# Optimization experiments

Hardware: AMD Instinct MI355X
Metric: run time of the kernel (lower is better)

Reference implementation:

```python
import jax, jax.numpy as jnp
import numpy as np

IN_FEATURES = 4096
OUT_FEATURES = 11008
PACK_COLS = IN_FEATURES // 2
BATCH, SEQ = 2, 2048


def setup_inputs() -> dict:
    key = jax.random.key(0)
    k_x, k_w, k_s, k_b = jax.random.split(key, 4)
    x = jax.random.normal(k_x, (BATCH, SEQ, IN_FEATURES), dtype=jnp.float32)
    # packed uint8 values (two int4 nibbles per byte), stored as int32 in [0, 256)
    weight_packed = jax.random.randint(k_w, (OUT_FEATURES, PACK_COLS), 0, 256, dtype=jnp.int32)
    # per-output-row dequant scale (abs_max/7 in the original); small positive values
    scale = jax.random.uniform(k_s, (OUT_FEATURES,), dtype=jnp.float32, minval=0.001, maxval=0.02)
    bias = jax.random.normal(k_b, (OUT_FEATURES,), dtype=jnp.float32)
    return {"x": x, "weight_packed": weight_packed, "scale": scale, "bias": bias}


def _dequantize(weight_packed, scale):
    # low nibble stored first (even columns), high nibble second (odd columns)
    lo = (weight_packed & 15) - 8          # [out, pack_cols] int32 in [-8, 7]
    hi = ((weight_packed >> 4) & 15) - 8   # [out, pack_cols]
    # interleave lo/hi -> [out, 2*pack_cols] matching w[:, 0::2]=lo, w[:, 1::2]=hi
    w_int = jnp.stack([lo, hi], axis=-1).reshape(OUT_FEATURES, 2 * PACK_COLS)
    w_int = w_int[:, :IN_FEATURES]
    return w_int.astype(jnp.float32) * scale[:, None]  # [out, in] fp32


def reference(x, weight_packed, scale, bias):
    w = _dequantize(weight_packed, scale)                 # [out, in]
    # F.linear: x @ w.T + bias
    return jnp.einsum('bsi,oi->bso', x, w) + bias
```

## Files before the change

kernel.cpp:

```cpp
#include <hip/hip_runtime.h>
#include <hip/hip_fp16.h>

#define M_TOTAL 4096
#define N_TOTAL 11008
#define K_TOTAL 4096
#define KPACK   2048

typedef _Float16 f16x4 __attribute__((ext_vector_type(4)));
typedef _Float16 f16x8 __attribute__((ext_vector_type(8)));
typedef float    f32x4 __attribute__((ext_vector_type(4)));

__device__ __forceinline__ void load16_to_lds(const void* g, void* l) {
    __builtin_amdgcn_global_load_lds(
        (const __attribute__((address_space(1))) unsigned int*)g,
        (__attribute__((address_space(3))) unsigned int*)l,
        16, 0, 0);
}

__global__ __launch_bounds__(256)
void _Int4Linear_cvt_x(const float* __restrict__ x, _Float16* __restrict__ xf) {
    const size_t i = ((size_t)blockIdx.x * 256 + threadIdx.x) * 8;
    const float4 v0 = *(const float4*)(x + i);
    const float4 v1 = *(const float4*)(x + i + 4);
    f16x8 h = { (_Float16)v0.x, (_Float16)v0.y, (_Float16)v0.z, (_Float16)v0.w,
                (_Float16)v1.x, (_Float16)v1.y, (_Float16)v1.z, (_Float16)v1.w };
    *(f16x8*)(xf + i) = h;
}

__global__ __launch_bounds__(256)
void _Int4Linear_dequant_w(const int* __restrict__ wp, _Float16* __restrict__ wf) {
    const size_t i = ((size_t)blockIdx.x * 256 + threadIdx.x) * 4;
    const int4 p = *(const int4*)(wp + i);
    const int v[4] = { p.x, p.y, p.z, p.w };
    f16x8 h;
    #pragma unroll
    for (int j = 0; j < 4; ++j) {
        h[2 * j]     = (_Float16)(( v[j]       & 15) - 8);
        h[2 * j + 1] = (_Float16)(((v[j] >> 4) & 15) - 8);
    }
    *(f16x8*)(wf + i * 2) = h;
}

#define BM 256
#define BN 256
#define NKT 64

__global__ __launch_bounds__(512, 2)
void _Int4Linear_54631984005366_kernel(const _Float16* __restrict__ A,
                                       const _Float16* __restrict__ B,
                                       const float* __restrict__ scale,
                                       const float* __restrict__ bias,
                                       float*       __restrict__ out)
{
    extern __shared__ char sm[];
    char* const smA = sm;
    char* const smB = sm + 65536;

    const int t    = threadIdx.x;
    const int wave = t >> 6;
    const int lane = t & 63;
    const int l16  = lane & 15;
    const int quad = lane >> 4;
    const int wm   = wave >> 2;
    const int wn   = wave & 3;

    const int b0 = blockIdx.x;
    const int sw = (b0 & 7) * 86 + (b0 >> 3);
    const int mBase = (sw & 15) * BM;
    const int nBase = (sw >> 4) * BN;

    const int srow = wave * 16 + (lane >> 2);
    const int scol = (((lane & 3) ^ ((lane >> 3) & 3)) << 3);
    const _Float16* const Ab = A + (size_t)(mBase + srow) * K_TOTAL + scol;
    const _Float16* const Bb = B + (size_t)(nBase + srow) * K_TOTAL + scol;
    const int ldst = wave * 1024;

    const int chA  = (quad ^ ((l16 >> 1) & 3)) << 4;
    const int aoff = (wm * 128 + l16) * 64 + chA;
    const int boff = (wn * 64  + l16) * 64 + chA;

    f32x4 acc[8][4] = {};

    #pragma unroll
    for (int r = 0; r < 2; ++r) load16_to_lds(Ab + (size_t)r * 128 * K_TOTAL,      smA + r * 8192 + ldst);
    #pragma unroll
    for (int r = 0; r < 2; ++r) load16_to_lds(Bb + (size_t)r * 128 * K_TOTAL,      smB + r * 8192 + ldst);
    #pragma unroll
    for (int r = 0; r < 2; ++r) load16_to_lds(Ab + (size_t)r * 128 * K_TOTAL + 32, smA + 16384 + r * 8192 + ldst);
    #pragma unroll
    for (int r = 0; r < 2; ++r) load16_to_lds(Bb + (size_t)r * 128 * K_TOTAL + 32, smB + 16384 + r * 8192 + ldst);
    asm volatile("s_waitcnt vmcnt(4)" ::: "memory");
    __builtin_amdgcn_s_barrier();
    __builtin_amdgcn_sched_barrier(0);

    #pragma unroll 2
    for (int t0 = 0; t0 < NKT; ++t0) {
        const int par = (t0 & 1) * 2;
        const int nxp = ((t0 + 1) & 1) * 2;
        const int tn  = (t0 < NKT - 1) ? (t0 + 1) : t0;
        const int kn  = tn * 64;
        char* const Ac0 = smA + (par    ) * 16384;
        char* const Ac1 = smA + (par + 1) * 16384;
        char* const Bc0 = smB + (par    ) * 16384;
        char* const Bc1 = smB + (par + 1) * 16384;
        char* const An0 = smA + (nxp    ) * 16384;
        char* const An1 = smA + (nxp + 1) * 16384;
        char* const Bn0 = smB + (nxp    ) * 16384;
        char* const Bn1 = smB + (nxp + 1) * 16384;

        {
            #pragma unroll
            for (int r = 0; r < 2; ++r) load16_to_lds(Ab + (size_t)r * 128 * K_TOTAL + kn, An0 + r * 8192 + ldst);
            #pragma unroll
            for (int r = 0; r < 2; ++r) load16_to_lds(Bb + (size_t)r * 128 * K_TOTAL + kn, Bn0 + r * 8192 + ldst);
            f16x8 a[8], b[4];
            #pragma unroll
            for (int f = 0; f < 8; ++f) a[f] = *(const f16x8*)(Ac0 + aoff + f * 1024);
            #pragma unroll
            for (int f = 0; f < 4; ++f) b[f] = *(const f16x8*)(Bc0 + boff + f * 1024);
            __builtin_amdgcn_s_setprio(1);
            #pragma unroll
            for (int mf = 0; mf < 8; ++mf)
                #pragma unroll
                for (int nf = 0; nf < 4; ++nf)
                    acc[mf][nf] = __builtin_amdgcn_mfma_f32_16x16x32_f16(a[mf], b[nf], acc[mf][nf], 0, 0, 0);
            __builtin_amdgcn_s_setprio(0);
            asm volatile("s_waitcnt vmcnt(4)" ::: "memory");
            __builtin_amdgcn_s_barrier();
            __builtin_amdgcn_sched_barrier(0);
        }

        {
            #pragma unroll
            for (int r = 0; r < 2; ++r) load16_to_lds(Ab + (size_t)r * 128 * K_TOTAL + kn + 32, An1 + r * 8192 + ldst);
            #pragma unroll
            for (int r = 0; r < 2; ++r) load16_to_lds(Bb + (size_t)r * 128 * K_TOTAL + kn + 32, Bn1 + r * 8192 + ldst);
            f16x8 a[8], b[4];
            #pragma unroll
            for (int f = 0; f < 8; ++f) a[f] = *(const f16x8*)(Ac1 + aoff + f * 1024);
            #pragma unroll
            for (int f = 0; f < 4; ++f) b[f] = *(const f16x8*)(Bc1 + boff + f * 1024);
            __builtin_amdgcn_s_setprio(1);
            #pragma unroll
            for (int mf = 0; mf < 8; ++mf)
                #pragma unroll
                for (int nf = 0; nf < 4; ++nf)
                    acc[mf][nf] = __builtin_amdgcn_mfma_f32_16x16x32_f16(a[mf], b[nf], acc[mf][nf], 0, 0, 0);
            __builtin_amdgcn_s_setprio(0);
            asm volatile("s_waitcnt vmcnt(4)" ::: "memory");
            __builtin_amdgcn_s_barrier();
            __builtin_amdgcn_sched_barrier(0);
        }
    }
    asm volatile("s_waitcnt vmcnt(0)" ::: "memory");

    #pragma unroll
    for (int nf = 0; nf < 4; ++nf) {
        const int n = nBase + wn * 64 + nf * 16 + l16;
        const float s  = scale[n];
        const float bz = bias[n];
        #pragma unroll
        for (int mf = 0; mf < 8; ++mf) {
            const int mb = mBase + wm * 128 + mf * 16 + quad * 4;
            #pragma unroll
            for (int r = 0; r < 4; ++r)
                out[(size_t)(mb + r) * N_TOTAL + n] = acc[mf][nf][r] * s + bz;
        }
    }
}

#define FBM 128
#define FBN 128
#define FBK 32
#define LDR 40
__global__ __launch_bounds__(256)
void _Int4Linear_fallback(const float* __restrict__ x, const int* __restrict__ wp,
                          const float* __restrict__ scale, const float* __restrict__ bias,
                          float* __restrict__ out)
{
    __shared__ _Float16 As[FBM * LDR];
    __shared__ _Float16 Bs[FBN * LDR];
    const int t = threadIdx.x, wave = t >> 6, lane = t & 63;
    const int l16 = lane & 15, quad = lane >> 4;
    const int nBase = blockIdx.x * FBN, mBase = blockIdx.y * FBM;
    const int wm = (wave >> 1) * 64, wn = (wave & 1) * 64;
    f32x4 acc[4][4] = {};
    for (int k0 = 0; k0 < K_TOTAL; k0 += FBK) {
        #pragma unroll
        for (int i = 0; i < 4; ++i) {
            const int li = i * 256 + t, row = li >> 3, c4 = li & 7;
            const float4 v = *(const float4*)(&x[(size_t)(mBase + row) * K_TOTAL + k0 + c4 * 4]);
            f16x4 hv = { (_Float16)v.x, (_Float16)v.y, (_Float16)v.z, (_Float16)v.w };
            *(f16x4*)(&As[row * LDR + c4 * 4]) = hv;
        }
        #pragma unroll
        for (int i = 0; i < 2; ++i) {
            const int li = i * 256 + t, row = li >> 2, c4 = li & 3;
            const int4 p = *(const int4*)(&wp[(size_t)(nBase + row) * KPACK + (k0 >> 1) + c4 * 4]);
            const int vals[4] = { p.x, p.y, p.z, p.w };
            f16x8 hv;
            #pragma unroll
            for (int j = 0; j < 4; ++j) {
                hv[2 * j]     = (_Float16)(( vals[j]       & 15) - 8);
                hv[2 * j + 1] = (_Float16)(((vals[j] >> 4) & 15) - 8);
            }
            *(f16x8*)(&Bs[row * LDR + c4 * 8]) = hv;
        }
        __syncthreads();
        f16x8 a[4], b[4];
        #pragma unroll
        for (int mt = 0; mt < 4; ++mt)
            a[mt] = *(const f16x8*)(&As[(wm + mt * 16 + l16) * LDR + quad * 8]);
        #pragma unroll
        for (int nt = 0; nt < 4; ++nt)
            b[nt] = *(const f16x8*)(&Bs[(wn + nt * 16 + l16) * LDR + quad * 8]);
        #pragma unroll
        for (int mt = 0; mt < 4; ++mt)
            #pragma unroll
            for (int nt = 0; nt < 4; ++nt)
                acc[mt][nt] = __builtin_amdgcn_mfma_f32_16x16x32_f16(a[mt], b[nt], acc[mt][nt], 0, 0, 0);
        __syncthreads();
    }
    #pragma unroll
    for (int nt = 0; nt < 4; ++nt) {
        const int n = nBase + wn + nt * 16 + l16;
        const float s = scale[n], bz = bias[n];
        #pragma unroll
        for (int mt = 0; mt < 4; ++mt)
            #pragma unroll
            for (int r = 0; r < 4; ++r)
                out[(size_t)(mBase + wm + mt * 16 + quad * 4 + r) * N_TOTAL + n] = acc[mt][nt][r] * s + bz;
    }
}

extern "C" void kernel_launch(void* const* d_in, const int* in_sizes, int n_in,
                              void* d_out, int out_size, void* d_ws, size_t ws_size,
                              hipStream_t stream) {
    const float* x     = (const float*)d_in[0];
    const int*   wp    = (const int*)d_in[1];
    const float* scale = (const float*)d_in[2];
    const float* bias  = (const float*)d_in[3];
    float*       out   = (float*)d_out;

    const size_t xf_bytes = (size_t)M_TOTAL * K_TOTAL * 2;
    const size_t wf_bytes = (size_t)N_TOTAL * K_TOTAL * 2;

    static int lds_attr_state = 0;
    if (lds_attr_state == 0) {
        hipError_t e = hipFuncSetAttribute(
            (const void*)_Int4Linear_54631984005366_kernel,
            hipFuncAttributeMaxDynamicSharedMemorySize, 131072);
        lds_attr_state = (e == hipSuccess) ? 1 : -1;
    }

    if (ws_size >= xf_bytes + wf_bytes && lds_attr_state == 1) {
        _Float16* xf = (_Float16*)d_ws;
        _Float16* wf = (_Float16*)((char*)d_ws + xf_bytes);
        _Int4Linear_cvt_x<<<8192, 256, 0, stream>>>(x, xf);
        _Int4Linear_dequant_w<<<22016, 256, 0, stream>>>(wp, wf);
        _Int4Linear_54631984005366_kernel<<<dim3(688), dim3(512), 131072, stream>>>(xf, wf, scale, bias, out);
    } else {
        dim3 grid(N_TOTAL / FBN, M_TOTAL / FBM);
        _Int4Linear_fallback<<<grid, 256, 0, stream>>>(x, wp, scale, bias, out);
    }
}
```

Measured before the change: 620.7 us.

## Load B fragments directly from global into registers, stage only A in LDS

The GEMM kernel stops staging the weight tile B through LDS. Each wave now reads its B MFMA fragments straight from global memory into double-buffered registers one phase ahead, and only A stays in a 4-slot LDS ring. This halves the LDS footprint to 64 KB and removes the B LDS writes and reads. The cost is uncoalesced 16-byte-per-lane global reads of B, repeated across the two wm waves, plus more registers and global latency exposed on the MFMA path.

```diff
diff --git a/kernel.cpp b/kernel.cpp
--- a/kernel.cpp
+++ b/kernel.cpp
@@ -45,6 +45,36 @@
 #define BN 256
 #define NKT 64
 
+__device__ __forceinline__ void gphase(const char* slotR, char* slotW,
+                                       f16x8 (&bcur)[4], f16x8 (&bnxt)[4],
+                                       const _Float16* Bf0, const _Float16* Bf1,
+                                       const _Float16* Bf2, const _Float16* Bf3,
+                                       int koffB,
+                                       const _Float16* Ab, int koffS, int ldst, int aoff,
+                                       f32x4 (&acc)[8][4])
+{
+    bnxt[0] = *(const f16x8*)(Bf0 + koffB);
+    bnxt[1] = *(const f16x8*)(Bf1 + koffB);
+    bnxt[2] = *(const f16x8*)(Bf2 + koffB);
+    bnxt[3] = *(const f16x8*)(Bf3 + koffB);
+    load16_to_lds(Ab + koffS,                             slotW + ldst);
+    load16_to_lds(Ab + (size_t)128 * K_TOTAL + koffS,     slotW + 8192 + ldst);
+    f16x8 a[8];
+    #pragma unroll
+    for (int f = 0; f < 8; ++f) a[f] = *(const f16x8*)(slotR + aoff + f * 1024);
+    asm volatile("s_waitcnt vmcnt(6)" ::: "memory");
+    __builtin_amdgcn_sched_barrier(0);
+    __builtin_amdgcn_s_setprio(1);
+    #pragma unroll
+    for (int mf = 0; mf < 8; ++mf)
+        #pragma unroll
+        for (int nf = 0; nf < 4; ++nf)
+            acc[mf][nf] = __builtin_amdgcn_mfma_f32_16x16x32_f16(a[mf], bcur[nf], acc[mf][nf], 0, 0, 0);
+    __builtin_amdgcn_s_setprio(0);
+    __builtin_amdgcn_s_barrier();
+    __builtin_amdgcn_sched_barrier(0);
+}
+
 __global__ __launch_bounds__(512, 2)
 void _Int4Linear_54631984005366_kernel(const _Float16* __restrict__ A,
                                        const _Float16* __restrict__ B,
@@ -53,8 +83,10 @@
                                        float*       __restrict__ out)
 {
     extern __shared__ char sm[];
-    char* const smA = sm;
-    char* const smB = sm + 65536;
+    char* const slot0 = sm;
+    char* const slot1 = sm + 16384;
+    char* const slot2 = sm + 32768;
+    char* const slot3 = sm + 49152;
 
     const int t    = threadIdx.x;
     const int wave = t >> 6;
@@ -72,85 +104,41 @@
     const int srow = wave * 16 + (lane >> 2);
     const int scol = (((lane & 3) ^ ((lane >> 3) & 3)) << 3);
     const _Float16* const Ab = A + (size_t)(mBase + srow) * K_TOTAL + scol;
-    const _Float16* const Bb = B + (size_t)(nBase + srow) * K_TOTAL + scol;
     const int ldst = wave * 1024;
 
     const int chA  = (quad ^ ((l16 >> 1) & 3)) << 4;
     const int aoff = (wm * 128 + l16) * 64 + chA;
-    const int boff = (wn * 64  + l16) * 64 + chA;
+
+    const _Float16* const Bf0 = B + (size_t)(nBase + wn * 64 +  0 + l16) * K_TOTAL + quad * 8;
+    const _Float16* const Bf1 = B + (size_t)(nBase + wn * 64 + 16 + l16) * K_TOTAL + quad * 8;
+    const _Float16* const Bf2 = B + (size_t)(nBase + wn * 64 + 32 + l16) * K_TOTAL + quad * 8;
+    const _Float16* const Bf3 = B + (size_t)(nBase + wn * 64 + 48 + l16) * K_TOTAL + quad * 8;
 
     f32x4 acc[8][4] = {};
-
-    #pragma unroll
-    for (int r = 0; r < 2; ++r) load16_to_lds(Ab + (size_t)r * 128 * K_TOTAL,      smA + r * 8192 + ldst);
-    #pragma unroll
-    for (int r = 0; r < 2; ++r) load16_to_lds(Bb + (size_t)r * 128 * K_TOTAL,      smB + r * 8192 + ldst);
-    #pragma unroll
-    for (int r = 0; r < 2; ++r) load16_to_lds(Ab + (size_t)r * 128 * K_TOTAL + 32, smA + 16384 + r * 8192 + ldst);
-    #pragma unroll
-    for (int r = 0; r < 2; ++r) load16_to_lds(Bb + (size_t)r * 128 * K_TOTAL + 32, smB + 16384 + r * 8192 + ldst);
-    asm volatile("s_waitcnt vmcnt(4)" ::: "memory");
+    f16x8 bA[4], bB[4];
+
+    bA[0] = *(const f16x8*)(Bf0);
+    bA[1] = *(const f16x8*)(Bf1);
+    bA[2] = *(const f16x8*)(Bf2);
+    bA[3] = *(const f16x8*)(Bf3);
+    #pragma unroll
+    for (int r = 0; r < 2; ++r) load16_to_lds(Ab + (size_t)r * 128 * K_TOTAL,      slot0 + r * 8192 + ldst);
+    #pragma unroll
+    for (int r = 0; r < 2; ++r) load16_to_lds(Ab + (size_t)r * 128 * K_TOTAL + 32, slot1 + r * 8192 + ldst);
+    asm volatile("s_waitcnt vmcnt(0)" ::: "memory");
     __builtin_amdgcn_s_barrier();
     __builtin_amdgcn_sched_barrier(0);
 
-    #pragma unroll 2
-    for (int t0 = 0; t0 < NKT; ++t0) {
-        const int par = (t0 & 1) * 2;
-        const int nxp = ((t0 + 1) & 1) * 2;
-        const int tn  = (t0 < NKT - 1) ? (t0 + 1) : t0;
-        const int kn  = tn * 64;
-        char* const Ac0 = smA + (par    ) * 16384;
-        char* const Ac1 = smA + (par + 1) * 16384;
-        char* const Bc0 = smB + (par    ) * 16384;
-        char* const Bc1 = smB + (par + 1) * 16384;
-        char* const An0 = smA + (nxp    ) * 16384;
-        char* const An1 = smA + (nxp + 1) * 16384;
-        char* const Bn0 = smB + (nxp    ) * 16384;
-        char* const Bn1 = smB + (nxp + 1) * 16384;
-
-        {
-            #pragma unroll
-            for (int r = 0; r < 2; ++r) load16_to_lds(Ab + (size_t)r * 128 * K_TOTAL + kn, An0 + r * 8192 + ldst);
-            #pragma unroll
-            for (int r = 0; r < 2; ++r) load16_to_lds(Bb + (size_t)r * 128 * K_TOTAL + kn, Bn0 + r * 8192 + ldst);
-            f16x8 a[8], b[4];
-            #pragma unroll
-            for (int f = 0; f < 8; ++f) a[f] = *(const f16x8*)(Ac0 + aoff + f * 1024);
-            #pragma unroll
-            for (int f = 0; f < 4; ++f) b[f] = *(const f16x8*)(Bc0 + boff + f * 1024);
-            __builtin_amdgcn_s_setprio(1);
-            #pragma unroll
-            for (int mf = 0; mf < 8; ++mf)
-                #pragma unroll
-                for (int nf = 0; nf < 4; ++nf)
-                    acc[mf][nf] = __builtin_amdgcn_mfma_f32_16x16x32_f16(a[mf], b[nf], acc[mf][nf], 0, 0, 0);
-            __builtin_amdgcn_s_setprio(0);
-            asm volatile("s_waitcnt vmcnt(4)" ::: "memory");
-            __builtin_amdgcn_s_barrier();
-            __builtin_amdgcn_sched_barrier(0);
-        }
-
-        {
-            #pragma unroll
-            for (int r = 0; r < 2; ++r) load16_to_lds(Ab + (size_t)r * 128 * K_TOTAL + kn + 32, An1 + r * 8192 + ldst);
-            #pragma unroll
-            for (int r = 0; r < 2; ++r) load16_to_lds(Bb + (size_t)r * 128 * K_TOTAL + kn + 32, Bn1 + r * 8192 + ldst);
-            f16x8 a[8], b[4];
-            #pragma unroll
-            for (int f = 0; f < 8; ++f) a[f] = *(const f16x8*)(Ac1 + aoff + f * 1024);
-            #pragma unroll
-            for (int f = 0; f < 4; ++f) b[f] = *(const f16x8*)(Bc1 + boff + f * 1024);
-            __builtin_amdgcn_s_setprio(1);
-            #pragma unroll
-            for (int mf = 0; mf < 8; ++mf)
-                #pragma unroll
-                for (int nf = 0; nf < 4; ++nf)
-                    acc[mf][nf] = __builtin_amdgcn_mfma_f32_16x16x32_f16(a[mf], b[nf], acc[mf][nf], 0, 0, 0);
-            __builtin_amdgcn_s_setprio(0);
-            asm volatile("s_waitcnt vmcnt(4)" ::: "memory");
-            __builtin_amdgcn_s_barrier();
-            __builtin_amdgcn_sched_barrier(0);
-        }
+    for (int t0 = 0; t0 < NKT; t0 += 2) {
+        const int ts2 = (t0 + 2 < NKT) ? t0 + 2 : NKT - 1;
+        gphase(slot0, slot2, bA, bB, Bf0, Bf1, Bf2, Bf3, t0 * 64 + 32,
+               Ab, (t0 + 1) * 64,      ldst, aoff, acc);
+        gphase(slot1, slot3, bB, bA, Bf0, Bf1, Bf2, Bf3, (t0 + 1) * 64,
+               Ab, (t0 + 1) * 64 + 32, ldst, aoff, acc);
+        gphase(slot2, slot0, bA, bB, Bf0, Bf1, Bf2, Bf3, (t0 + 1) * 64 + 32,
+               Ab, ts2 * 64,           ldst, aoff, acc);
+        gphase(slot3, slot1, bB, bA, Bf0, Bf1, Bf2, Bf3, ts2 * 64,
+               Ab, ts2 * 64 + 32,      ldst, aoff, acc);
     }
     asm volatile("s_waitcnt vmcnt(0)" ::: "memory");
 
@@ -249,7 +237,7 @@
     if (lds_attr_state == 0) {
         hipError_t e = hipFuncSetAttribute(
             (const void*)_Int4Linear_54631984005366_kernel,
-            hipFuncAttributeMaxDynamicSharedMemorySize, 131072);
+            hipFuncAttributeMaxDynamicSharedMemorySize, 65536);
         lds_attr_state = (e == hipSuccess) ? 1 : -1;
     }
 
@@ -258,7 +246,7 @@
         _Float16* wf = (_Float16*)((char*)d_ws + xf_bytes);
         _Int4Linear_cvt_x<<<8192, 256, 0, stream>>>(x, xf);
         _Int4Linear_dequant_w<<<22016, 256, 0, stream>>>(wp, wf);
-        _Int4Linear_54631984005366_kernel<<<dim3(688), dim3(512), 131072, stream>>>(xf, wf, scale, bias, out);
+        _Int4Linear_54631984005366_kernel<<<dim3(688), dim3(512), 65536, stream>>>(xf, wf, scale, bias, out);
     } else {
         dim3 grid(N_TOTAL / FBN, M_TOTAL / FBM);
         _Int4Linear_fallback<<<grid, 256, 0, stream>>>(x, wp, scale, bias, out);
```

After: 830.9 us. +33.9%, slower.

## Register double-buffer A fragments and interleave loads with MFMAs via sched groups

Applied to the files above, without the earlier changes.

Restructures the K loop so the A fragments for the next half-tile are read from LDS into a second register set while the current MFMAs run. All eight global-to-LDS loads for the next tile are now issued in the first half-step. sched_group_barrier hints interleave VMEM, LDS reads and MFMAs. This aims to hide LDS read latency behind MFMA work, but it raises register pressure and waits on vmcnt(0) mid-iteration, which leaves less time for global loads to overlap.

```diff
diff --git a/kernel.cpp b/kernel.cpp
--- a/kernel.cpp
+++ b/kernel.cpp
@@ -9,6 +9,11 @@
 typedef _Float16 f16x4 __attribute__((ext_vector_type(4)));
 typedef _Float16 f16x8 __attribute__((ext_vector_type(8)));
 typedef float    f32x4 __attribute__((ext_vector_type(4)));
+
+#define SGB(mask, n) __builtin_amdgcn_sched_group_barrier((mask), (n), 0)
+#define SG_MFMA  0x008
+#define SG_VMEM  0x010
+#define SG_DSRD  0x100
 
 __device__ __forceinline__ void load16_to_lds(const void* g, void* l) {
     __builtin_amdgcn_global_load_lds(
@@ -80,74 +85,72 @@
     const int boff = (wn * 64  + l16) * 64 + chA;
 
     f32x4 acc[8][4] = {};
-
-    #pragma unroll
-    for (int r = 0; r < 2; ++r) load16_to_lds(Ab + (size_t)r * 128 * K_TOTAL,      smA + r * 8192 + ldst);
-    #pragma unroll
-    for (int r = 0; r < 2; ++r) load16_to_lds(Bb + (size_t)r * 128 * K_TOTAL,      smB + r * 8192 + ldst);
-    #pragma unroll
-    for (int r = 0; r < 2; ++r) load16_to_lds(Ab + (size_t)r * 128 * K_TOTAL + 32, smA + 16384 + r * 8192 + ldst);
-    #pragma unroll
-    for (int r = 0; r < 2; ++r) load16_to_lds(Bb + (size_t)r * 128 * K_TOTAL + 32, smB + 16384 + r * 8192 + ldst);
-    asm volatile("s_waitcnt vmcnt(4)" ::: "memory");
+    f16x8 a0[8], a1[8], b[4];
+
+    load16_to_lds(Ab,                                smA + ldst);
+    load16_to_lds(Ab + (size_t)128 * K_TOTAL,        smA + 8192 + ldst);
+    load16_to_lds(Bb,                                smB + ldst);
+    load16_to_lds(Bb + (size_t)128 * K_TOTAL,        smB + 8192 + ldst);
+    load16_to_lds(Ab + 32,                           smA + 16384 + ldst);
+    load16_to_lds(Ab + (size_t)128 * K_TOTAL + 32,   smA + 16384 + 8192 + ldst);
+    load16_to_lds(Bb + 32,                           smB + 16384 + ldst);
+    load16_to_lds(Bb + (size_t)128 * K_TOTAL + 32,   smB + 16384 + 8192 + ldst);
+    asm volatile("s_waitcnt vmcnt(0)" ::: "memory");
     __builtin_amdgcn_s_barrier();
     __builtin_amdgcn_sched_barrier(0);
-
-    #pragma unroll 2
+    #pragma unroll
+    for (int f = 0; f < 8; ++f) a0[f] = *(const f16x8*)(smA + aoff + f * 1024);
+
     for (int t0 = 0; t0 < NKT; ++t0) {
         const int par = (t0 & 1) * 2;
-        const int nxp = ((t0 + 1) & 1) * 2;
-        const int tn  = (t0 < NKT - 1) ? (t0 + 1) : t0;
+        const int nx  = ((t0 + 1) & 1) * 2;
+        const int tn  = (t0 < NKT - 1) ? (t0 + 1) : NKT - 1;
         const int kn  = tn * 64;
-        char* const Ac0 = smA + (par    ) * 16384;
-        char* const Ac1 = smA + (par + 1) * 16384;
-        char* const Bc0 = smB + (par    ) * 16384;
-        char* const Bc1 = smB + (par + 1) * 16384;
-        char* const An0 = smA + (nxp    ) * 16384;
-        char* const An1 = smA + (nxp + 1) * 16384;
-        char* const Bn0 = smB + (nxp    ) * 16384;
-        char* const Bn1 = smB + (nxp + 1) * 16384;
+        char* const AcP = smA + par * 16384;
+        (void)AcP;
 
         {
-            #pragma unroll
-            for (int r = 0; r < 2; ++r) load16_to_lds(Ab + (size_t)r * 128 * K_TOTAL + kn, An0 + r * 8192 + ldst);
-            #pragma unroll
-            for (int r = 0; r < 2; ++r) load16_to_lds(Bb + (size_t)r * 128 * K_TOTAL + kn, Bn0 + r * 8192 + ldst);
-            f16x8 a[8], b[4];
-            #pragma unroll
-            for (int f = 0; f < 8; ++f) a[f] = *(const f16x8*)(Ac0 + aoff + f * 1024);
-            #pragma unroll
-            for (int f = 0; f < 4; ++f) b[f] = *(const f16x8*)(Bc0 + boff + f * 1024);
+            load16_to_lds(Ab + kn,                              smA + nx * 16384 + ldst);
+            load16_to_lds(Ab + (size_t)128 * K_TOTAL + kn,      smA + nx * 16384 + 8192 + ldst);
+            load16_to_lds(Bb + kn,                              smB + nx * 16384 + ldst);
+            load16_to_lds(Bb + (size_t)128 * K_TOTAL + kn,      smB + nx * 16384 + 8192 + ldst);
+            load16_to_lds(Ab + kn + 32,                         smA + (nx + 1) * 16384 + ldst);
+            load16_to_lds(Ab + (size_t)128 * K_TOTAL + kn + 32, smA + (nx + 1) * 16384 + 8192 + ldst);
+            load16_to_lds(Bb + kn + 32,                         smB + (nx + 1) * 16384 + ldst);
+            load16_to_lds(Bb + (size_t)128 * K_TOTAL + kn + 32, smB + (nx + 1) * 16384 + 8192 + ldst);
+            #pragma unroll
+            for (int f = 0; f < 4; ++f) b[f] = *(const f16x8*)(smB + par * 16384 + boff + f * 1024);
+            #pragma unroll
+            for (int f = 0; f < 8; ++f) a1[f] = *(const f16x8*)(smA + (par + 1) * 16384 + aoff + f * 1024);
             __builtin_amdgcn_s_setprio(1);
             #pragma unroll
             for (int mf = 0; mf < 8; ++mf)
                 #pragma unroll
                 for (int nf = 0; nf < 4; ++nf)
-                    acc[mf][nf] = __builtin_amdgcn_mfma_f32_16x16x32_f16(a[mf], b[nf], acc[mf][nf], 0, 0, 0);
+                    acc[mf][nf] = __builtin_amdgcn_mfma_f32_16x16x32_f16(a0[mf], b[nf], acc[mf][nf], 0, 0, 0);
             __builtin_amdgcn_s_setprio(0);
-            asm volatile("s_waitcnt vmcnt(4)" ::: "memory");
+            SGB(SG_VMEM, 8);
+            SGB(SG_DSRD, 4); SGB(SG_MFMA, 8);
+            SGB(SG_DSRD, 8); SGB(SG_MFMA, 24);
+            asm volatile("s_waitcnt vmcnt(0)" ::: "memory");
             __builtin_amdgcn_s_barrier();
             __builtin_amdgcn_sched_barrier(0);
         }
 
         {
             #pragma unroll
-            for (int r = 0; r < 2; ++r) load16_to_lds(Ab + (size_t)r * 128 * K_TOTAL + kn + 32, An1 + r * 8192 + ldst);
-            #pragma unroll
-            for (int r = 0; r < 2; ++r) load16_to_lds(Bb + (size_t)r * 128 * K_TOTAL + kn + 32, Bn1 + r * 8192 + ldst);
-            f16x8 a[8], b[4];
-            #pragma unroll
-            for (int f = 0; f < 8; ++f) a[f] = *(const f16x8*)(Ac1 + aoff + f * 1024);
-            #pragma unroll
-            for (int f = 0; f < 4; ++f) b[f] = *(const f16x8*)(Bc1 + boff + f * 1024);
+            for (int f = 0; f < 4; ++f) b[f] = *(const f16x8*)(smB + (par + 1) * 16384 + boff + f * 1024);
+            #pragma unroll
+            for (int f = 0; f < 8; ++f) a0[f] = *(const f16x8*)(smA + nx * 16384 + aoff + f * 1024);
             __builtin_amdgcn_s_setprio(1);
             #pragma unroll
             for (int mf = 0; mf < 8; ++mf)
                 #pragma unroll
                 for (int nf = 0; nf < 4; ++nf)
-                    acc[mf][nf] = __builtin_amdgcn_mfma_f32_16x16x32_f16(a[mf], b[nf], acc[mf][nf], 0, 0, 0);
+                    acc[mf][nf] = __builtin_amdgcn_mfma_f32_16x16x32_f16(a1[mf], b[nf], acc[mf][nf], 0, 0, 0);
             __builtin_amdgcn_s_setprio(0);
-            asm volatile("s_waitcnt vmcnt(4)" ::: "memory");
+            SGB(SG_DSRD, 4); SGB(SG_MFMA, 8);
+            SGB(SG_DSRD, 8); SGB(SG_MFMA, 24);
             __builtin_amdgcn_s_barrier();
             __builtin_amdgcn_sched_barrier(0);
         }
```

After: 755.0 us. +21.6%, slower.

## Switch GEMM to 32x32x16 MFMA tiles and merge prep kernels into one launch

Applied to the files above, without the earlier changes.

The main GEMM now issues 32x32x16 f16 MFMA instructions over a 4x2 grid of 32x32 accumulator tiles per wave, replacing the 8x4 grid of 16x16x32 tiles. LDS fragment addressing and the epilogue row mapping are rewritten to match the 32x32 output layout. This cuts the instruction count and uses a larger MFMA shape that may give higher throughput, at the cost of a different LDS read pattern whose bank-conflict behaviour under the existing swizzle is unclear. Separately, the x conversion and weight dequant kernels are fused into one launch to remove a kernel boundary.

```diff
diff --git a/kernel.cpp b/kernel.cpp
--- a/kernel.cpp
+++ b/kernel.cpp
@@ -6,9 +6,10 @@
 #define K_TOTAL 4096
 #define KPACK   2048
 
-typedef _Float16 f16x4 __attribute__((ext_vector_type(4)));
-typedef _Float16 f16x8 __attribute__((ext_vector_type(8)));
-typedef float    f32x4 __attribute__((ext_vector_type(4)));
+typedef _Float16 f16x4  __attribute__((ext_vector_type(4)));
+typedef _Float16 f16x8  __attribute__((ext_vector_type(8)));
+typedef float    f32x4  __attribute__((ext_vector_type(4)));
+typedef float    f32x16 __attribute__((ext_vector_type(16)));
 
 __device__ __forceinline__ void load16_to_lds(const void* g, void* l) {
     __builtin_amdgcn_global_load_lds(
@@ -18,27 +19,28 @@
 }
 
 __global__ __launch_bounds__(256)
-void _Int4Linear_cvt_x(const float* __restrict__ x, _Float16* __restrict__ xf) {
-    const size_t i = ((size_t)blockIdx.x * 256 + threadIdx.x) * 8;
-    const float4 v0 = *(const float4*)(x + i);
-    const float4 v1 = *(const float4*)(x + i + 4);
-    f16x8 h = { (_Float16)v0.x, (_Float16)v0.y, (_Float16)v0.z, (_Float16)v0.w,
-                (_Float16)v1.x, (_Float16)v1.y, (_Float16)v1.z, (_Float16)v1.w };
-    *(f16x8*)(xf + i) = h;
-}
-
-__global__ __launch_bounds__(256)
-void _Int4Linear_dequant_w(const int* __restrict__ wp, _Float16* __restrict__ wf) {
-    const size_t i = ((size_t)blockIdx.x * 256 + threadIdx.x) * 4;
-    const int4 p = *(const int4*)(wp + i);
-    const int v[4] = { p.x, p.y, p.z, p.w };
-    f16x8 h;
-    #pragma unroll
-    for (int j = 0; j < 4; ++j) {
-        h[2 * j]     = (_Float16)(( v[j]       & 15) - 8);
-        h[2 * j + 1] = (_Float16)(((v[j] >> 4) & 15) - 8);
-    }
-    *(f16x8*)(wf + i * 2) = h;
+void _Int4Linear_prep(const float* __restrict__ x, _Float16* __restrict__ xf,
+                      const int* __restrict__ wp, _Float16* __restrict__ wf) {
+    const int bid = blockIdx.x;
+    if (bid < 8192) {
+        const size_t i = ((size_t)bid * 256 + threadIdx.x) * 8;
+        const float4 v0 = *(const float4*)(x + i);
+        const float4 v1 = *(const float4*)(x + i + 4);
+        f16x8 h = { (_Float16)v0.x, (_Float16)v0.y, (_Float16)v0.z, (_Float16)v0.w,
+                    (_Float16)v1.x, (_Float16)v1.y, (_Float16)v1.z, (_Float16)v1.w };
+        *(f16x8*)(xf + i) = h;
+    } else {
+        const size_t i = ((size_t)(bid - 8192) * 256 + threadIdx.x) * 4;
+        const int4 p = *(const int4*)(wp + i);
+        const int v[4] = { p.x, p.y, p.z, p.w };
+        f16x8 h;
+        #pragma unroll
+        for (int j = 0; j < 4; ++j) {
+            h[2 * j]     = (_Float16)(( v[j]       & 15) - 8);
+            h[2 * j + 1] = (_Float16)(((v[j] >> 4) & 15) - 8);
+        }
+        *(f16x8*)(wf + i * 2) = h;
+    }
 }
 
 #define BM 256
@@ -59,8 +61,8 @@
     const int t    = threadIdx.x;
     const int wave = t >> 6;
     const int lane = t & 63;
-    const int l16  = lane & 15;
-    const int quad = lane >> 4;
+    const int l31  = lane & 31;
+    const int h    = lane >> 5;
     const int wm   = wave >> 2;
     const int wn   = wave & 3;
 
@@ -75,11 +77,13 @@
     const _Float16* const Bb = B + (size_t)(nBase + srow) * K_TOTAL + scol;
     const int ldst = wave * 1024;
 
-    const int chA  = (quad ^ ((l16 >> 1) & 3)) << 4;
-    const int aoff = (wm * 128 + l16) * 64 + chA;
-    const int boff = (wn * 64  + l16) * 64 + chA;
-
-    f32x4 acc[8][4] = {};
+    const int sA    = (l31 >> 1) & 3;
+    const int aBase = (wm * 128 + l31) * 64;
+    const int bBase = (wn * 64  + l31) * 64;
+    const int pc0   = ((0 * 2 + h) ^ sA) << 4;
+    const int pc1   = ((1 * 2 + h) ^ sA) << 4;
+
+    f32x16 acc[4][2] = {};
 
     #pragma unroll
     for (int r = 0; r < 2; ++r) load16_to_lds(Ab + (size_t)r * 128 * K_TOTAL,      smA + r * 8192 + ldst);
@@ -113,17 +117,23 @@
             for (int r = 0; r < 2; ++r) load16_to_lds(Ab + (size_t)r * 128 * K_TOTAL + kn, An0 + r * 8192 + ldst);
             #pragma unroll
             for (int r = 0; r < 2; ++r) load16_to_lds(Bb + (size_t)r * 128 * K_TOTAL + kn, Bn0 + r * 8192 + ldst);
-            f16x8 a[8], b[4];
-            #pragma unroll
-            for (int f = 0; f < 8; ++f) a[f] = *(const f16x8*)(Ac0 + aoff + f * 1024);
-            #pragma unroll
-            for (int f = 0; f < 4; ++f) b[f] = *(const f16x8*)(Bc0 + boff + f * 1024);
+            f16x8 a[4][2], b[2][2];
+            b[0][0] = *(const f16x8*)(Bc0 + bBase + pc0);
+            #pragma unroll
+            for (int mb = 0; mb < 4; ++mb) a[mb][0] = *(const f16x8*)(Ac0 + aBase + mb * 2048 + pc0);
+            b[1][0] = *(const f16x8*)(Bc0 + bBase + 2048 + pc0);
+            b[0][1] = *(const f16x8*)(Bc0 + bBase + pc1);
+            b[1][1] = *(const f16x8*)(Bc0 + bBase + 2048 + pc1);
+            #pragma unroll
+            for (int mb = 0; mb < 4; ++mb) a[mb][1] = *(const f16x8*)(Ac0 + aBase + mb * 2048 + pc1);
             __builtin_amdgcn_s_setprio(1);
             #pragma unroll
-            for (int mf = 0; mf < 8; ++mf)
+            for (int ks = 0; ks < 2; ++ks)
                 #pragma unroll
-                for (int nf = 0; nf < 4; ++nf)
-                    acc[mf][nf] = __builtin_amdgcn_mfma_f32_16x16x32_f16(a[mf], b[nf], acc[mf][nf], 0, 0, 0);
+                for (int mb = 0; mb < 4; ++mb)
+                    #pragma unroll
+                    for (int nb = 0; nb < 2; ++nb)
+                        acc[mb][nb] = __builtin_amdgcn_mfma_f32_32x32x16_f16(a[mb][ks], b[nb][ks], acc[mb][nb], 0, 0, 0);
             __builtin_amdgcn_s_setprio(0);
             asm volatile("s_waitcnt vmcnt(4)" ::: "memory");
             __builtin_amdgcn_s_barrier();
@@ -135,17 +145,23 @@
             for (int r = 0; r < 2; ++r) load16_to_lds(Ab + (size_t)r * 128 * K_TOTAL + kn + 32, An1 + r * 8192 + ldst);
             #pragma unroll
             for (int r = 0; r < 2; ++r) load16_to_lds(Bb + (size_t)r * 128 * K_TOTAL + kn + 32, Bn1 + r * 8192 + ldst);
-            f16x8 a[8], b[4];
-            #pragma unroll
-            for (int f = 0; f < 8; ++f) a[f] = *(const f16x8*)(Ac1 + aoff + f * 1024);
-            #pragma unroll
-            for (int f = 0; f < 4; ++f) b[f] = *(const f16x8*)(Bc1 + boff + f * 1024);
+            f16x8 a[4][2], b[2][2];
+            b[0][0] = *(const f16x8*)(Bc1 + bBase + pc0);
+            #pragma unroll
+            for (int mb = 0; mb < 4; ++mb) a[mb][0] = *(const f16x8*)(Ac1 + aBase + mb * 2048 + pc0);
+            b[1][0] = *(const f16x8*)(Bc1 + bBase + 2048 + pc0);
+            b[0][1] = *(const f16x8*)(Bc1 + bBase + pc1);
+            b[1][1] = *(const f16x8*)(Bc1 + bBase + 2048 + pc1);
+            #pragma unroll
+            for (int mb = 0; mb < 4; ++mb) a[mb][1] = *(const f16x8*)(Ac1 + aBase + mb * 2048 + pc1);
             __builtin_amdgcn_s_setprio(1);
             #pragma unroll
-            for (int mf = 0; mf < 8; ++mf)
+            for (int ks = 0; ks < 2; ++ks)
                 #pragma unroll
-                for (int nf = 0; nf < 4; ++nf)
-                    acc[mf][nf] = __builtin_amdgcn_mfma_f32_16x16x32_f16(a[mf], b[nf], acc[mf][nf], 0, 0, 0);
+                for (int mb = 0; mb < 4; ++mb)
+                    #pragma unroll
+                    for (int nb = 0; nb < 2; ++nb)
+                        acc[mb][nb] = __builtin_amdgcn_mfma_f32_32x32x16_f16(a[mb][ks], b[nb][ks], acc[mb][nb], 0, 0, 0);
             __builtin_amdgcn_s_setprio(0);
             asm volatile("s_waitcnt vmcnt(4)" ::: "memory");
             __builtin_amdgcn_s_barrier();
@@ -155,16 +171,18 @@
     asm volatile("s_waitcnt vmcnt(0)" ::: "memory");
 
     #pragma unroll
-    for (int nf = 0; nf < 4; ++nf) {
-        const int n = nBase + wn * 64 + nf * 16 + l16;
+    for (int nb = 0; nb < 2; ++nb) {
+        const int n = nBase + wn * 64 + nb * 32 + l31;
         const float s  = scale[n];
         const float bz = bias[n];
         #pragma unroll
-        for (int mf = 0; mf < 8; ++mf) {
-            const int mb = mBase + wm * 128 + mf * 16 + quad * 4;
-            #pragma unroll
-            for (int r = 0; r < 4; ++r)
-                out[(size_t)(mb + r) * N_TOTAL + n] = acc[mf][nf][r] * s + bz;
+        for (int mb = 0; mb < 4; ++mb) {
+            const int mb0 = mBase + wm * 128 + mb * 32 + 4 * h;
+            #pragma unroll
+            for (int i = 0; i < 16; ++i) {
+                const int m = mb0 + (i & 3) + 8 * (i >> 2);
+                out[(size_t)m * N_TOTAL + n] = acc[mb][nb][i] * s + bz;
+            }
         }
     }
 }
@@ -256,8 +274,7 @@
     if (ws_size >= xf_bytes + wf_bytes && lds_attr_state == 1) {
         _Float16* xf = (_Float16*)d_ws;
         _Float16* wf = (_Float16*)((char*)d_ws + xf_bytes);
-        _Int4Linear_cvt_x<<<8192, 256, 0, stream>>>(x, xf);
-        _Int4Linear_dequant_w<<<22016, 256, 0, stream>>>(wp, wf);
+        _Int4Linear_prep<<<30208, 256, 0, stream>>>(x, xf, wp, wf);
         _Int4Linear_54631984005366_kernel<<<dim3(688), dim3(512), 131072, stream>>>(xf, wf, scale, bias, out);
     } else {
         dim3 grid(N_TOTAL / FBN, M_TOTAL / FBM);
```

After: 644.3 us. 3.8% more time.
